# Optimization experiments

Measured on AMD Instinct MI355X. Metric: run time of the kernel, lower is better.

The kernel has to match this reference:

```python
import jax, jax.numpy as jnp
import numpy as np


def setup_inputs() -> dict:
    key = jax.random.key(0)
    k1, k2 = jax.random.split(key)
    B, Q, K, H = 8, 2048, 2048, 128
    out_state = jax.random.normal(k1, (B, Q, H), dtype=jnp.float32)
    history = jax.random.normal(k2, (B, K, H), dtype=jnp.float32)
    return {"out_state": out_state, "history": history}


def reference(out_state, history):
    # tanh pre-activation on queries
    q = jnp.tanh(out_state)                              # [B, Q, H]
    # unscaled QK^T scores
    scores = jnp.einsum("bqh,bkh->bqk", q, history)      # [B, Q, K]
    probs = jax.nn.softmax(scores, axis=2)               # softmax over keys
    attn = jnp.einsum("bqk,bkh->bqh", probs, history)    # [B, Q, H]
    return attn
```

## Files before the change

### kernel.cpp

```cpp
#include <hip/hip_runtime.h>
#include <math.h>


typedef _Float16 half8  __attribute__((ext_vector_type(8)));
typedef _Float16 half4  __attribute__((ext_vector_type(4)));
typedef __fp16   fp16x2 __attribute__((ext_vector_type(2)));
typedef float    f32x4  __attribute__((ext_vector_type(4)));
typedef float    f32x2  __attribute__((ext_vector_type(2)));
typedef float    f32x16 __attribute__((ext_vector_type(16)));

#define QQ 2048
#define KK 2048
#define HH 128
#define BM 64
#define BN 64
#define NTILES 32
#define L2E 1.44269504f

#define KH_HALVES      ((size_t)8 * KK * HH)
#define PREP_BYTES     (KH_HALVES * 4)
#define OSPLIT_BYTES   ((size_t)256 * BM * HH * 2)
#define MLSPLIT_FLOATS ((size_t)256 * BM)

union U32H { unsigned int u; _Float16 h[2]; };
union U64H { unsigned long long u; _Float16 h[4]; };
union H2I  { fp16x2 h; int i; };
union I4H8 { int i[4]; half8 h; };

typedef __attribute__((address_space(1))) const void gvoid;
typedef __attribute__((address_space(3))) void lvoid;

#define WAITVM8 asm volatile("s_waitcnt vmcnt(8)" ::: "memory")
#define WAITVM0 asm volatile("s_waitcnt vmcnt(0)" ::: "memory")
static __device__ __forceinline__ void wgbar() {
    asm volatile("" ::: "memory");
    __builtin_amdgcn_s_barrier();
    asm volatile("" ::: "memory");
}

__launch_bounds__(256)
__global__ void attn_prep_k(const float* __restrict__ history,
                            _Float16* __restrict__ wsh) {
    __shared__ __align__(16) _Float16 Ks[BN * HH];
    __shared__ __align__(16) _Float16 Vt[HH * BN];

    const int tid = threadIdx.x;
    const int bid = blockIdx.x;
    const int b   = bid >> 5;
    const int kt  = bid & 31;

    const float* hb = history + ((size_t)b * KK + (size_t)kt * BN) * HH;
    const int r0 = tid >> 5;
    const int c4 = (tid & 31) * 4;
    #pragma unroll
    for (int j = 0; j < 8; ++j) {
        const int k = r0 + 8 * j;
        const float4 g = *(const float4*)(hb + (size_t)k * HH + c4);
        half4 hv;
        hv[0] = (_Float16)g.x; hv[1] = (_Float16)g.y;
        hv[2] = (_Float16)g.z; hv[3] = (_Float16)g.w;
        *(half4*)&Ks[k * HH + (c4 ^ ((k & 7) << 3))] = hv;
    }
    __syncthreads();

    {
        const int h0  = 2 * (tid & 63);
        const int n0t = (tid >> 6) * 16;
        half8 ra0, ra1, rb0, rb1;
        #pragma unroll
        for (int i = 0; i < 8; ++i) {
            const int n = n0t + i;
            U32H t; t.u = *(const unsigned int*)&Ks[n * HH + (h0 ^ ((n & 7) << 3))];
            ra0[i] = t.h[0]; rb0[i] = t.h[1];
        }
        #pragma unroll
        for (int i = 8; i < 16; ++i) {
            const int n = n0t + i;
            U32H t; t.u = *(const unsigned int*)&Ks[n * HH + (h0 ^ ((n & 7) << 3))];
            ra1[i - 8] = t.h[0]; rb1[i - 8] = t.h[1];
        }
        const int th0 = (h0 & 7) << 3;
        const int th1 = ((h0 + 1) & 7) << 3;
        *(half8*)&Vt[(h0    ) * BN + ((n0t    ) ^ th0)] = ra0;
        *(half8*)&Vt[(h0    ) * BN + ((n0t + 8) ^ th0)] = ra1;
        *(half8*)&Vt[(h0 + 1) * BN + ((n0t    ) ^ th1)] = rb0;
        *(half8*)&Vt[(h0 + 1) * BN + ((n0t + 8) ^ th1)] = rb1;
    }
    __syncthreads();

    _Float16* kdst = wsh + ((size_t)b * KK + (size_t)kt * BN) * HH;
    _Float16* vdst = wsh + KH_HALVES + ((size_t)(b * NTILES + kt)) * (HH * BN);
    const f32x4* ksrc = (const f32x4*)Ks;
    const f32x4* vsrc = (const f32x4*)Vt;
    #pragma unroll
    for (int i = 0; i < 4; ++i) {
        ((f32x4*)kdst)[i * 256 + tid] = ksrc[i * 256 + tid];
        ((f32x4*)vdst)[i * 256 + tid] = vsrc[i * 256 + tid];
    }
}

__launch_bounds__(128, 2)
__global__ void attn_main_k(const float* __restrict__ out_state,
                            const _Float16* __restrict__ wsh,
                            float* __restrict__ out,
                            char* __restrict__ wsb,
                            int splits) {
    __shared__ __align__(16) _Float16 KsL[BN * HH];
    __shared__ __align__(16) _Float16 VtL[HH * BN];

    const int tid  = threadIdx.x;
    const int wave = tid >> 6;
    const int lane = tid & 63;
    const int l31  = lane & 31;
    const int hi   = lane >> 5;
    const int swzk = (lane & 7) << 3;

    const int nwg  = gridDim.x;
    const int cpx  = nwg >> 3;
    const int work = (blockIdx.x & 7) * cpx + (blockIdx.x >> 3);
    const int s    = work >> 8;
    const int r256 = work & 255;
    const int b    = r256 >> 5;
    const int qb   = r256 & 31;
    const int q    = qb * BM + wave * 32 + l31;

    const int kt0 = (NTILES * s) / splits;
    const int kt1 = (NTILES * (s + 1)) / splits;

    const _Float16* khb = wsh + (size_t)b * KK * HH;
    const _Float16* vtb = wsh + KH_HALVES + (size_t)b * NTILES * (HH * BN);

    auto issueK = [&](int t) {
        const char* g = (const char*)(khb + (size_t)t * (BN * HH));
        #pragma unroll
        for (int c = 0; c < 8; ++c) {
            const int off = (c * 2 + wave) * 1024 + lane * 16;
            __builtin_amdgcn_global_load_lds((gvoid*)(g + off),
                                             (lvoid*)((char*)KsL + off), 16, 0, 0);
        }
    };
    auto issueV = [&](int t) {
        const char* g = (const char*)(vtb + (size_t)t * (HH * BN));
        #pragma unroll
        for (int c = 0; c < 8; ++c) {
            const int off = (c * 2 + wave) * 1024 + lane * 16;
            __builtin_amdgcn_global_load_lds((gvoid*)(g + off),
                                             (lvoid*)((char*)VtL + off), 16, 0, 0);
        }
    };

    float4 qa[16];
    {
        const float* qrow = out_state + ((size_t)b * QQ + q) * HH;
        #pragma unroll
        for (int hs = 0; hs < 8; ++hs) {
            qa[2 * hs]     = *(const float4*)(qrow + hs * 16 + hi * 8);
            qa[2 * hs + 1] = *(const float4*)(qrow + hs * 16 + hi * 8 + 4);
        }
    }
    issueK(kt0);
    issueV(kt0);

    auto th = [](float x) {
        const float e = __builtin_amdgcn_exp2f(x * (2.0f * L2E));
        return 1.0f - 2.0f * __builtin_amdgcn_rcpf(e + 1.0f);
    };
    half8 qf[8];
    #pragma unroll
    for (int hs = 0; hs < 8; ++hs) {
        const float4 a = qa[2 * hs], c = qa[2 * hs + 1];
        qf[hs][0] = (_Float16)th(a.x); qf[hs][1] = (_Float16)th(a.y);
        qf[hs][2] = (_Float16)th(a.z); qf[hs][3] = (_Float16)th(a.w);
        qf[hs][4] = (_Float16)th(c.x); qf[hs][5] = (_Float16)th(c.y);
        qf[hs][6] = (_Float16)th(c.z); qf[hs][7] = (_Float16)th(c.w);
    }

    f32x16 O[4];
    #pragma unroll
    for (int i = 0; i < 4; ++i)
        #pragma unroll
        for (int r = 0; r < 16; ++r) O[i][r] = 0.f;
    float Osum = 0.f;
    float rmax = -3.0e38f;

    for (int kt = kt0; kt < kt1; ++kt) {
        const bool more = (kt + 1 < kt1);

        WAITVM8;
        wgbar();

        f32x16 S0, S1;
        #pragma unroll
        for (int r = 0; r < 16; ++r) { S0[r] = 0.f; S1[r] = 0.f; }
        __builtin_amdgcn_s_setprio(1);
        #pragma unroll
        for (int hs = 0; hs < 8; ++hs) {
            const int col = (hs * 16 + hi * 8) ^ swzk;
            const half8 k0 = *(const half8*)&KsL[l31 * 128 + col];
            const half8 k1 = *(const half8*)&KsL[(l31 + 32) * 128 + col];
            S0 = __builtin_amdgcn_mfma_f32_32x32x16_f16(k0, qf[hs], S0, 0, 0, 0);
            S1 = __builtin_amdgcn_mfma_f32_32x32x16_f16(k1, qf[hs], S1, 0, 0, 0);
        }
        __builtin_amdgcn_s_setprio(0);

        wgbar();
        if (more) issueK(kt + 1);

        float tmax = S0[0];
        #pragma unroll
        for (int r = 1; r < 16; ++r) tmax = fmaxf(tmax, S0[r]);
        #pragma unroll
        for (int r = 0; r < 16; ++r) tmax = fmaxf(tmax, S1[r]);
        tmax = fmaxf(tmax, __shfl_xor(tmax, 32, 64));

        if (!__all(tmax <= rmax)) {
            const float nm    = fmaxf(rmax, tmax);
            const float alpha = __builtin_amdgcn_exp2f((rmax - nm) * L2E);
            rmax = nm;
            #pragma unroll
            for (int i = 0; i < 4; ++i) O[i] *= alpha;
            Osum *= alpha;
        }

        #pragma unroll
        for (int r = 0; r < 16; ++r) S0[r] = __builtin_amdgcn_exp2f((S0[r] - rmax) * L2E);
        #pragma unroll
        for (int r = 0; r < 16; ++r) S1[r] = __builtin_amdgcn_exp2f((S1[r] - rmax) * L2E);

        float ls = 0.f;
        #pragma unroll
        for (int r = 0; r < 16; ++r) ls += S0[r] + S1[r];
        Osum += ls + __shfl_xor(ls, 32, 64);

        int d0[8], d1[8];
        #pragma unroll
        for (int M = 0; M < 8; ++M) {
            const int r0 = (M & 3) * 4;
            H2I u0, u1;
            if (M < 4) {
                u0.h = __builtin_amdgcn_cvt_pkrtz(S0[r0], S0[r0 + 1]);
                u1.h = __builtin_amdgcn_cvt_pkrtz(S0[r0 + 2], S0[r0 + 3]);
            } else {
                u0.h = __builtin_amdgcn_cvt_pkrtz(S1[r0], S1[r0 + 1]);
                u1.h = __builtin_amdgcn_cvt_pkrtz(S1[r0 + 2], S1[r0 + 3]);
            }
            d0[M] = u0.i; d1[M] = u1.i;
        }

        if (more) { WAITVM8; } else { WAITVM0; }
        wgbar();

        __builtin_amdgcn_s_setprio(1);
        #pragma unroll
        for (int ns = 0; ns < 4; ++ns) {
            const int x  = d0[2 * ns],     x2 = d1[2 * ns];
            const int y  = d0[2 * ns + 1], y2 = d1[2 * ns + 1];
            const int px  = __shfl_xor(x, 32, 64),  px2 = __shfl_xor(x2, 32, 64);
            const int py  = __shfl_xor(y, 32, 64),  py2 = __shfl_xor(y2, 32, 64);
            I4H8 bf;
            bf.i[0] = hi ? py  : x;
            bf.i[1] = hi ? py2 : x2;
            bf.i[2] = hi ? y   : px;
            bf.i[3] = hi ? y2  : px2;
            #pragma unroll
            for (int ht = 0; ht < 4; ++ht) {
                const half8 vf = *(const half8*)
                    &VtL[(ht * 32 + l31) * 64 + ((ns * 16 + hi * 8) ^ swzk)];
                O[ht] = __builtin_amdgcn_mfma_f32_32x32x16_f16(vf, bf.h, O[ht], 0, 0, 0);
            }
        }
        __builtin_amdgcn_s_setprio(0);

        wgbar();
        if (more) issueV(kt + 1);
    }

    if (splits == 1) {
        const float inv = 1.0f / Osum;
        float* orow = out + ((size_t)b * QQ + q) * HH;
        #pragma unroll
        for (int ht = 0; ht < 4; ++ht)
            #pragma unroll
            for (int m = 0; m < 4; ++m) {
                f32x4 v;
                v[0] = O[ht][4 * m]     * inv; v[1] = O[ht][4 * m + 1] * inv;
                v[2] = O[ht][4 * m + 2] * inv; v[3] = O[ht][4 * m + 3] * inv;
                *(f32x4*)&orow[ht * 32 + 8 * m + 4 * hi] = v;
            }
    } else {
        const float inv = 1.0f / Osum;
        _Float16* oh = (_Float16*)(wsb + PREP_BYTES)
                     + ((size_t)(s * 256 + r256) * BM + wave * 32 + l31) * HH;
        #pragma unroll
        for (int ht = 0; ht < 4; ++ht)
            #pragma unroll
            for (int m = 0; m < 4; ++m) {
                half4 hv;
                hv[0] = (_Float16)(O[ht][4 * m]     * inv);
                hv[1] = (_Float16)(O[ht][4 * m + 1] * inv);
                hv[2] = (_Float16)(O[ht][4 * m + 2] * inv);
                hv[3] = (_Float16)(O[ht][4 * m + 3] * inv);
                *(half4*)&oh[ht * 32 + 8 * m + 4 * hi] = hv;
            }
        if (!hi) {
            float* wm = (float*)(wsb + PREP_BYTES + (size_t)splits * OSPLIT_BYTES);
            const size_t idx = (size_t)(s * 256 + r256) * BM + wave * 32 + l31;
            wm[idx] = rmax;
            wm[(size_t)splits * MLSPLIT_FLOATS + idx] = Osum;
        }
    }
}

template<int SPL>
__launch_bounds__(256)
__global__ void attn_combine_k(const char* __restrict__ wsb,
                               float* __restrict__ out) {
    const int idx = blockIdx.x * 256 + threadIdx.x;
    const int h4  = idx & 31;
    const int q   = (idx >> 5) & 2047;
    const int b   = idx >> 16;
    const int blk = b * 32 + (q >> 6);
    const int qr  = q & 63;

    const _Float16* oh = (const _Float16*)(wsb + PREP_BYTES);
    const float* wm = (const float*)(wsb + PREP_BYTES + (size_t)SPL * OSPLIT_BYTES);
    const float* wl = wm + (size_t)SPL * MLSPLIT_FLOATS;

    float ms[SPL];
    float M = -3.0e38f;
    #pragma unroll
    for (int s = 0; s < SPL; ++s) {
        ms[s] = wm[(size_t)(s * 256 + blk) * BM + qr];
        M = fmaxf(M, ms[s]);
    }
    float denom = 0.f;
    float v0 = 0.f, v1 = 0.f, v2 = 0.f, v3 = 0.f;
    #pragma unroll
    for (int s = 0; s < SPL; ++s) {
        const float wgt = exp2f((ms[s] - M) * L2E) * wl[(size_t)(s * 256 + blk) * BM + qr];
        denom += wgt;
        U64H t;
        t.u = *(const unsigned long long*)&oh[(size_t)(s * 256 + blk) * (BM * HH)
                                              + (size_t)qr * HH + 4 * h4];
        v0 += wgt * (float)t.h[0];
        v1 += wgt * (float)t.h[1];
        v2 += wgt * (float)t.h[2];
        v3 += wgt * (float)t.h[3];
    }
    const float inv = 1.0f / denom;
    f32x4 r; r[0] = v0 * inv; r[1] = v1 * inv; r[2] = v2 * inv; r[3] = v3 * inv;
    *(f32x4*)&out[((size_t)(b * QQ + q)) * HH + 4 * h4] = r;
}

extern "C" void kernel_launch(void* const* d_in, const int* in_sizes, int n_in,
                              void* d_out, int out_size, void* d_ws, size_t ws_size,
                              hipStream_t stream) {
    const float* out_state = (const float*)d_in[0];
    const float* history   = (const float*)d_in[1];
    float* out = (float*)d_out;
    char* wsb  = (char*)d_ws;

    const size_t need4 = PREP_BYTES + 4 * OSPLIT_BYTES + 4 * 2 * MLSPLIT_FLOATS * 4;
    const size_t need3 = PREP_BYTES + 3 * OSPLIT_BYTES + 3 * 2 * MLSPLIT_FLOATS * 4;
    const int splits = (ws_size >= need4) ? 4 : (ws_size >= need3) ? 3 : 1;

    attn_prep_k<<<dim3(256), dim3(256), 0, stream>>>(history, (_Float16*)wsb);
    attn_main_k<<<dim3(256 * splits), dim3(128), 0, stream>>>(out_state, (const _Float16*)wsb,
                                                              out, wsb, splits);
    if (splits == 4)
        attn_combine_k<4><<<dim3(2048), dim3(256), 0, stream>>>(wsb, out);
    else if (splits == 3)
        attn_combine_k<3><<<dim3(2048), dim3(256), 0, stream>>>(wsb, out);
}
```

Before: 108.4 us.

## Double-buffer K/V tiles in LDS and widen workgroups to 128 query rows

The main attention kernel now uses 4 waves (256 threads) per workgroup, covering 128 query rows instead of 64. Each K/V tile loaded into LDS is therefore shared by twice as many queries, and the grid is halved. K and V LDS buffers are double-buffered: the next tile's loads are issued right after the barrier, before the current tile's MFMAs. This removes one barrier per phase and overlaps global-to-LDS transfers with compute. The cost is doubled LDS per block (64KB), which may reduce occupancy, and fewer workgroups to spread across CUs.

```diff
diff --git a/kernel.cpp b/kernel.cpp
--- a/kernel.cpp
+++ b/kernel.cpp
@@ -6,21 +6,20 @@
 typedef _Float16 half4  __attribute__((ext_vector_type(4)));
 typedef __fp16   fp16x2 __attribute__((ext_vector_type(2)));
 typedef float    f32x4  __attribute__((ext_vector_type(4)));
-typedef float    f32x2  __attribute__((ext_vector_type(2)));
 typedef float    f32x16 __attribute__((ext_vector_type(16)));
 
 #define QQ 2048
 #define KK 2048
 #define HH 128
-#define BM 64
+#define QBM 128
 #define BN 64
 #define NTILES 32
 #define L2E 1.44269504f
 
 #define KH_HALVES      ((size_t)8 * KK * HH)
 #define PREP_BYTES     (KH_HALVES * 4)
-#define OSPLIT_BYTES   ((size_t)256 * BM * HH * 2)
-#define MLSPLIT_FLOATS ((size_t)256 * BM)
+#define OSPLIT_BYTES   ((size_t)128 * QBM * HH * 2)
+#define MLSPLIT_FLOATS ((size_t)128 * QBM)
 
 union U32H { unsigned int u; _Float16 h[2]; };
 union U64H { unsigned long long u; _Float16 h[4]; };
@@ -30,7 +29,7 @@
 typedef __attribute__((address_space(1))) const void gvoid;
 typedef __attribute__((address_space(3))) void lvoid;
 
-#define WAITVM8 asm volatile("s_waitcnt vmcnt(8)" ::: "memory")
+#define WAITVM4 asm volatile("s_waitcnt vmcnt(4)" ::: "memory")
 #define WAITVM0 asm volatile("s_waitcnt vmcnt(0)" ::: "memory")
 static __device__ __forceinline__ void wgbar() {
     asm volatile("" ::: "memory");
@@ -99,14 +98,14 @@
     }
 }
 
-__launch_bounds__(128, 2)
+__launch_bounds__(256, 2)
 __global__ void attn_main_k(const float* __restrict__ out_state,
                             const _Float16* __restrict__ wsh,
                             float* __restrict__ out,
                             char* __restrict__ wsb,
                             int splits) {
-    __shared__ __align__(16) _Float16 KsL[BN * HH];
-    __shared__ __align__(16) _Float16 VtL[HH * BN];
+    __shared__ __align__(16) _Float16 KsL[2][BN * HH];
+    __shared__ __align__(16) _Float16 VtL[2][HH * BN];
 
     const int tid  = threadIdx.x;
     const int wave = tid >> 6;
@@ -118,11 +117,11 @@
     const int nwg  = gridDim.x;
     const int cpx  = nwg >> 3;
     const int work = (blockIdx.x & 7) * cpx + (blockIdx.x >> 3);
-    const int s    = work >> 8;
-    const int r256 = work & 255;
-    const int b    = r256 >> 5;
-    const int qb   = r256 & 31;
-    const int q    = qb * BM + wave * 32 + l31;
+    const int s    = work >> 7;
+    const int r128 = work & 127;
+    const int b    = r128 >> 4;
+    const int qb   = r128 & 15;
+    const int q    = qb * QBM + wave * 32 + l31;
 
     const int kt0 = (NTILES * s) / splits;
     const int kt1 = (NTILES * (s + 1)) / splits;
@@ -130,22 +129,22 @@
     const _Float16* khb = wsh + (size_t)b * KK * HH;
     const _Float16* vtb = wsh + KH_HALVES + (size_t)b * NTILES * (HH * BN);
 
-    auto issueK = [&](int t) {
+    auto issueK = [&](int t, int pb) {
         const char* g = (const char*)(khb + (size_t)t * (BN * HH));
         #pragma unroll
-        for (int c = 0; c < 8; ++c) {
-            const int off = (c * 2 + wave) * 1024 + lane * 16;
+        for (int c = 0; c < 4; ++c) {
+            const int off = (c * 4 + wave) * 1024 + lane * 16;
             __builtin_amdgcn_global_load_lds((gvoid*)(g + off),
-                                             (lvoid*)((char*)KsL + off), 16, 0, 0);
+                                             (lvoid*)((char*)KsL[pb] + off), 16, 0, 0);
         }
     };
-    auto issueV = [&](int t) {
+    auto issueV = [&](int t, int pb) {
         const char* g = (const char*)(vtb + (size_t)t * (HH * BN));
         #pragma unroll
-        for (int c = 0; c < 8; ++c) {
-            const int off = (c * 2 + wave) * 1024 + lane * 16;
+        for (int c = 0; c < 4; ++c) {
+            const int off = (c * 4 + wave) * 1024 + lane * 16;
             __builtin_amdgcn_global_load_lds((gvoid*)(g + off),
-                                             (lvoid*)((char*)VtL + off), 16, 0, 0);
+                                             (lvoid*)((char*)VtL[pb] + off), 16, 0, 0);
         }
     };
 
@@ -158,8 +157,8 @@
             qa[2 * hs + 1] = *(const float4*)(qrow + hs * 16 + hi * 8 + 4);
         }
     }
-    issueK(kt0);
-    issueV(kt0);
+    issueK(kt0, 0);
+    issueV(kt0, 0);
 
     auto th = [](float x) {
         const float e = __builtin_amdgcn_exp2f(x * (2.0f * L2E));
@@ -184,10 +183,12 @@
     float rmax = -3.0e38f;
 
     for (int kt = kt0; kt < kt1; ++kt) {
+        const int  pb   = kt & 1;
         const bool more = (kt + 1 < kt1);
 
-        WAITVM8;
+        WAITVM4;
         wgbar();
+        if (more) issueK(kt + 1, pb ^ 1);
 
         f32x16 S0, S1;
         #pragma unroll
@@ -196,15 +197,12 @@
         #pragma unroll
         for (int hs = 0; hs < 8; ++hs) {
             const int col = (hs * 16 + hi * 8) ^ swzk;
-            const half8 k0 = *(const half8*)&KsL[l31 * 128 + col];
-            const half8 k1 = *(const half8*)&KsL[(l31 + 32) * 128 + col];
+            const half8 k0 = *(const half8*)&KsL[pb][l31 * 128 + col];
+            const half8 k1 = *(const half8*)&KsL[pb][(l31 + 32) * 128 + col];
             S0 = __builtin_amdgcn_mfma_f32_32x32x16_f16(k0, qf[hs], S0, 0, 0, 0);
             S1 = __builtin_amdgcn_mfma_f32_32x32x16_f16(k1, qf[hs], S1, 0, 0, 0);
         }
         __builtin_amdgcn_s_setprio(0);
-
-        wgbar();
-        if (more) issueK(kt + 1);
 
         float tmax = S0[0];
         #pragma unroll
@@ -247,8 +245,9 @@
             d0[M] = u0.i; d1[M] = u1.i;
         }
 
-        if (more) { WAITVM8; } else { WAITVM0; }
+        if (more) { WAITVM4; } else { WAITVM0; }
         wgbar();
+        if (more) issueV(kt + 1, pb ^ 1);
 
         __builtin_amdgcn_s_setprio(1);
         #pragma unroll
@@ -265,14 +264,11 @@
             #pragma unroll
             for (int ht = 0; ht < 4; ++ht) {
                 const half8 vf = *(const half8*)
-                    &VtL[(ht * 32 + l31) * 64 + ((ns * 16 + hi * 8) ^ swzk)];
+                    &VtL[pb][(ht * 32 + l31) * 64 + ((ns * 16 + hi * 8) ^ swzk)];
                 O[ht] = __builtin_amdgcn_mfma_f32_32x32x16_f16(vf, bf.h, O[ht], 0, 0, 0);
             }
         }
         __builtin_amdgcn_s_setprio(0);
-
-        wgbar();
-        if (more) issueV(kt + 1);
     }
 
     if (splits == 1) {
@@ -290,7 +286,7 @@
     } else {
         const float inv = 1.0f / Osum;
         _Float16* oh = (_Float16*)(wsb + PREP_BYTES)
-                     + ((size_t)(s * 256 + r256) * BM + wave * 32 + l31) * HH;
+                     + ((size_t)(s * 128 + r128) * QBM + wave * 32 + l31) * HH;
         #pragma unroll
         for (int ht = 0; ht < 4; ++ht)
             #pragma unroll
@@ -304,7 +300,7 @@
             }
         if (!hi) {
             float* wm = (float*)(wsb + PREP_BYTES + (size_t)splits * OSPLIT_BYTES);
-            const size_t idx = (size_t)(s * 256 + r256) * BM + wave * 32 + l31;
+            const size_t idx = (size_t)(s * 128 + r128) * QBM + wave * 32 + l31;
             wm[idx] = rmax;
             wm[(size_t)splits * MLSPLIT_FLOATS + idx] = Osum;
         }
@@ -319,8 +315,8 @@
     const int h4  = idx & 31;
     const int q   = (idx >> 5) & 2047;
     const int b   = idx >> 16;
-    const int blk = b * 32 + (q >> 6);
-    const int qr  = q & 63;
+    const int blk = b * 16 + (q >> 7);
+    const int qr  = q & 127;
 
     const _Float16* oh = (const _Float16*)(wsb + PREP_BYTES);
     const float* wm = (const float*)(wsb + PREP_BYTES + (size_t)SPL * OSPLIT_BYTES);
@@ -330,18 +326,18 @@
     float M = -3.0e38f;
     #pragma unroll
     for (int s = 0; s < SPL; ++s) {
-        ms[s] = wm[(size_t)(s * 256 + blk) * BM + qr];
+        ms[s] = wm[(size_t)(s * 128 + blk) * QBM + qr];
         M = fmaxf(M, ms[s]);
     }
     float denom = 0.f;
     float v0 = 0.f, v1 = 0.f, v2 = 0.f, v3 = 0.f;
     #pragma unroll
     for (int s = 0; s < SPL; ++s) {
-        const float wgt = exp2f((ms[s] - M) * L2E) * wl[(size_t)(s * 256 + blk) * BM + qr];
+        const float wgt = exp2f((ms[s] - M) * L2E) * wl[(size_t)(s * 128 + blk) * QBM + qr];
         denom += wgt;
         U64H t;
-        t.u = *(const unsigned long long*)&oh[(size_t)(s * 256 + blk) * (BM * HH)
-                                              + (size_t)qr * HH + 4 * h4];
+        t.u = *(const unsigned long long*)&oh[((size_t)(s * 128 + blk) * QBM + qr) * HH
+                                              + 4 * h4];
         v0 += wgt * (float)t.h[0];
         v1 += wgt * (float)t.h[1];
         v2 += wgt * (float)t.h[2];
@@ -365,7 +361,7 @@
     const int splits = (ws_size >= need4) ? 4 : (ws_size >= need3) ? 3 : 1;
 
     attn_prep_k<<<dim3(256), dim3(256), 0, stream>>>(history, (_Float16*)wsb);
-    attn_main_k<<<dim3(256 * splits), dim3(128), 0, stream>>>(out_state, (const _Float16*)wsb,
+    attn_main_k<<<dim3(128 * splits), dim3(256), 0, stream>>>(out_state, (const _Float16*)wsb,
                                                               out, wsb, splits);
     if (splits == 4)
         attn_combine_k<4><<<dim3(2048), dim3(256), 0, stream>>>(wsb, out);
```

Result: no change. 108.0 us (-0.4%).
